# Optimization experiments

Hardware: AMD Instinct MI355X
Metric: run time of the kernel (lower is better)

Reference implementation:

```python
import jax, jax.numpy as jnp
import numpy as np


def setup_inputs() -> dict:
    key = jax.random.key(0)
    k1, k2, k3, k4, k5, k6 = jax.random.split(key, 6)
    H = 1024
    B, La, Lq = 32, 512, 64
    # kaiming_uniform with a=sqrt(5) on [H,H]: bound = sqrt(6/((1+5)*H)) = 1/sqrt(H)
    bound = 1.0 / np.sqrt(H)
    return {
        "article_feature": jax.random.normal(k1, (B, La, H), dtype=jnp.float32),
        "query_op_feature": jax.random.normal(k2, (B, Lq, H), dtype=jnp.float32),
        "weight1_1": jax.random.uniform(k3, (H, H), minval=-bound, maxval=bound, dtype=jnp.float32),
        "weight1_2": jax.random.uniform(k4, (H, H), minval=-bound, maxval=bound, dtype=jnp.float32),
        "weight2_1": jax.random.uniform(k5, (H, H), minval=-bound, maxval=bound, dtype=jnp.float32),
        "weight2_2": jax.random.uniform(k6, (H, H), minval=-bound, maxval=bound, dtype=jnp.float32),
    }


def reference(article_feature, query_op_feature, weight1_1, weight1_2, weight2_1, weight2_2):
    # article_feature: [B, La, H], query_op_feature: [B, Lq, H]
    # aq_attention: softmax over Lq of (A @ W1_1) @ Q^T -> [B, La, Lq]
    aq_scores = jnp.einsum("bah,hk,bqk->baq", article_feature, weight1_1, query_op_feature)
    aq_attention = jax.nn.softmax(aq_scores, axis=2)
    # qa_attention: softmax over La of (Q @ W1_2) @ A^T -> [B, Lq, La]
    qa_scores = jnp.einsum("bqh,hk,bak->bqa", query_op_feature, weight1_2, article_feature)
    qa_attention = jax.nn.softmax(qa_scores, axis=2)
    # S_a: relu((aq_attention @ Q) @ W2_1) -> [B, La, H]
    S_a = jax.nn.relu(jnp.einsum("baq,bqh,hk->bak", aq_attention, query_op_feature, weight2_1))
    # S_q: relu((qa_attention @ A) @ W2_2) -> [B, Lq, H]
    S_q = jax.nn.relu(jnp.einsum("bqa,bah,hk->bqk", qa_attention, article_feature, weight2_2))
    S_aq = jnp.max(S_a, axis=1)  # [B, H]
    S_qa = jnp.max(S_q, axis=1)  # [B, H]
    g = jnp.float32(0.5)
    return g * S_aq + (1.0 - g) * S_qa
```

## Files before the change

kernel.cpp:

```cpp
#include <hip/hip_runtime.h>
#include <stdint.h>


using f16x8 = __attribute__((ext_vector_type(8))) _Float16;
using f32x4 = __attribute__((ext_vector_type(4))) float;
typedef const __attribute__((address_space(1))) void* gas_t;
typedef __attribute__((address_space(3))) void* las_t;

__device__ __forceinline__ unsigned short f2h(float x) {
  _Float16 h = (_Float16)x;
  return __builtin_bit_cast(unsigned short, h);
}


__global__ __launch_bounds__(256) void conv16(const float* __restrict__ in,
    unsigned short* __restrict__ hi)
{
  int i = blockIdx.x * 256 + threadIdx.x;
  float4 v = ((const float4*)in)[i];
  ushort4 h;
  h.x = f2h(v.x); h.y = f2h(v.y); h.z = f2h(v.z); h.w = f2h(v.w);
  ((ushort4*)hi)[i] = h;
}

__global__ __launch_bounds__(256) void prep_W(
    const float* __restrict__ W11, const float* __restrict__ W12,
    const float* __restrict__ W21, const float* __restrict__ W22,
    unsigned short* __restrict__ Wcat, unsigned short* __restrict__ W21T,
    unsigned short* __restrict__ W22T)
{
  __shared__ float tile[32][33];
  int z = blockIdx.z;
  const float* src = z == 0 ? W11 : z == 1 ? W12 : z == 2 ? W21 : W22;
  int r0 = blockIdx.y * 32, c0 = blockIdx.x * 32;
  int tx = threadIdx.x, ty = threadIdx.y;
  #pragma unroll
  for (int i = 0; i < 4; ++i) {
    int r = r0 + ty + i * 8;
    float v = src[(long)r * 1024 + c0 + tx];
    tile[ty + i * 8][tx] = v;
    if (z == 0) Wcat[(long)r * 1024 + c0 + tx] = f2h(v);
  }
  __syncthreads();
  if (z > 0) {
    #pragma unroll
    for (int i = 0; i < 4; ++i) {
      float v = tile[tx][ty + i * 8];
      long o = (long)(c0 + ty + i * 8) * 1024 + r0 + tx;
      if (z == 1)      Wcat[1048576 + o] = f2h(v);
      else if (z == 2) W21T[o] = f2h(v);
      else             W22T[o] = f2h(v);
    }
  }
}

template<int BM, int BN, int OUT, bool BF32>
__device__ __forceinline__ void gemm_body(
    char* smem, int bx, int by, int z,
    const unsigned short* __restrict__ Ah,
    const unsigned short* __restrict__ Bh, const float* __restrict__ Bf,
    float* __restrict__ Cf, unsigned short* __restrict__ Ch,
    int M, int N, int K, int ldA, int ldB, int ldC, long sA, long sB, long sC, int mtiles)
{
  constexpr int AB = BM * 64;
  constexpr int MI = BM / 32, NI = BN / 32;
  char* As = smem;
  char* Bs = smem + AB;

  const int m0 = by * BM, n0 = bx * BN;
  const int t = threadIdx.x, lane = t & 63;
  const int wid = t >> 6, wr = wid >> 1, wc = wid & 1;

  const unsigned short* Ab = Ah + (long)z * sA;
  const unsigned short* Bb = BF32 ? nullptr : Bh + (long)z * sB;
  const float* Bfb = BF32 ? Bf + (long)z * sB : nullptr;

  f32x4 acc[MI][NI];
  #pragma unroll
  for (int i = 0; i < MI; ++i)
    #pragma unroll
    for (int j = 0; j < NI; ++j)
      acc[i][j] = f32x4{0.f, 0.f, 0.f, 0.f};

  auto stage4k = [&](char* lbuf, const unsigned short* g, int ld, int row0, int k0, int rmax) {
    int ob = t * 16;
    int e  = ob ^ (((ob >> 7) & 3) << 4);
    int m  = e >> 6, k = (e & 63) >> 1;
    int row = row0 + m; row = row < rmax ? row : rmax - 1;
    const unsigned short* gp = g + (long)row * ld + k0 + k;
    char* lp = lbuf + (t & ~63) * 16;
    __builtin_amdgcn_global_load_lds((gas_t)(const void*)gp, (las_t)(void*)lp, 16, 0, 0);
  };
  auto stageB_f32 = [&](char* lbuf, const float* g, int ld, int nb, int k0) {
    int ob = t * 16;
    int e  = ob ^ (((ob >> 7) & 3) << 4);
    int n  = e >> 6, kb = (e & 63) >> 1;
    f16x8 pk;
    #pragma unroll
    for (int j = 0; j < 8; ++j) {
      float v = g[(long)(k0 + kb + j) * ld + nb + n];
      pk[j] = (_Float16)v;
    }
    *(f16x8*)(lbuf + ob) = pk;
  };
  auto ldfrag = [&](const char* lbuf, int rr) -> f16x8 {
    int ob = rr * 64 + (lane >> 4) * 16;
    ob ^= ((ob >> 7) & 3) << 4;
    return *(const f16x8*)(lbuf + ob);
  };

  for (int k0 = 0; k0 < K; k0 += 32) {
    stage4k(As, Ab, ldA, m0, k0, M);
    if (BM == 128) stage4k(As + 4096, Ab, ldA, m0 + 64, k0, M);
    if (BF32) {
      stageB_f32(Bs, Bfb, ldB, n0, k0);
    } else {
      stage4k(Bs, Bb, ldB, n0, k0, N);
      if (BN == 128) stage4k(Bs + 4096, Bb, ldB, n0 + 64, k0, N);
    }
    __syncthreads();

    f16x8 ah[MI];
    #pragma unroll
    for (int mi = 0; mi < MI; ++mi)
      ah[mi] = ldfrag(As, wr * (BM / 2) + mi * 16 + (lane & 15));
    #pragma unroll
    for (int ni = 0; ni < NI; ++ni) {
      f16x8 bh = ldfrag(Bs, wc * (BN / 2) + ni * 16 + (lane & 15));
      #pragma unroll
      for (int mi = 0; mi < MI; ++mi)
        acc[mi][ni] = __builtin_amdgcn_mfma_f32_16x16x32_f16(ah[mi], bh, acc[mi][ni], 0, 0, 0);
    }
    __syncthreads();
  }

  if (OUT == 4 || OUT == 5) {
    float* red = (float*)smem;
    #pragma unroll
    for (int ni = 0; ni < NI; ++ni) {
      float pm = 0.0f;
      #pragma unroll
      for (int mi = 0; mi < MI; ++mi)
        #pragma unroll
        for (int r = 0; r < 4; ++r)
          pm = fmaxf(pm, acc[mi][ni][r]);
      int g = wr * 4 + (lane >> 4);
      int col = wc * (BN / 2) + ni * 16 + (lane & 15);
      red[g * BN + col] = pm;
    }
    __syncthreads();
    if (OUT == 4) {
      if (t < BN) {
        float m = red[t];
        #pragma unroll
        for (int g = 1; g < 8; ++g) m = fmaxf(m, red[g * BN + t]);
        Cf[(long)(z * mtiles + by) * ldC + n0 + t] = m;
      }
    } else {
      constexpr int NGR = BM / 64, PG = 8 / NGR;
      if (t < NGR * BN) {
        int hh = t / BN, col = t - hh * BN;
        float m = red[(hh * PG) * BN + col];
        #pragma unroll
        for (int i = 1; i < PG; ++i) m = fmaxf(m, red[(hh * PG + i) * BN + col]);
        Cf[(long)((m0 >> 6) + hh) * ldC + n0 + col] = m;
      }
    }
    return;
  }

  #pragma unroll
  for (int mi = 0; mi < MI; ++mi) {
    #pragma unroll
    for (int r = 0; r < 4; ++r) {
      int grow = m0 + wr * (BM / 2) + mi * 16 + (lane >> 4) * 4 + r;
      #pragma unroll
      for (int ni = 0; ni < NI; ++ni) {
        int gcol = n0 + wc * (BN / 2) + ni * 16 + (lane & 15);
        float v = acc[mi][ni][r];
        if (OUT == 1) {
          int b = grow >> 6, q = grow & 63;
          long dst = (long)b * 131072 + (long)((gcol >> 10) * 64 + q) * 1024 + (gcol & 1023);
          Ch[dst] = f2h(v);
        } else if (OUT == 2) {
          if (grow < M) Ch[(long)z * sC + (long)grow * ldC + gcol] = f2h(v);
        } else if (OUT == 3) {
          long dst = (long)(grow >> 6) * 65536 + (long)gcol * 64 + (grow & 63);
          Ch[dst] = f2h(v);
        }
      }
    }
  }
}


__global__ __launch_bounds__(256) void g1_kernel(
    const unsigned short* Q_hi, const unsigned short* Wcat, const unsigned short* W21T,
    unsigned short* Pcat, unsigned short* P3T)
{
  __shared__ char smem[12288];
  int bid = blockIdx.x;
  if (bid < 512) {
    gemm_body<128, 64, 1, false>(smem, bid & 31, bid >> 5, 0,
        Q_hi, Wcat, nullptr, nullptr, Pcat,
        2048, 2048, 1024, 1024, 1024, 0, 0, 0, 0, 0);
  } else {
    int b2 = bid - 512;
    gemm_body<128, 64, 3, false>(smem, b2 & 15, b2 >> 4, 0,
        Q_hi, W21T, nullptr, nullptr, P3T,
        2048, 1024, 1024, 1024, 1024, 0, 0, 0, 0, 0);
  }
}


__global__ __launch_bounds__(512) void g2_kernel(
    const float* __restrict__ Afeat, const unsigned short* __restrict__ Pcat,
    float* __restrict__ Spar)
{
  __shared__ char smem[12288];
  char* Ash = smem;
  char* Bs  = smem + 4096;

  int orig = blockIdx.x;
  int xcd = orig & 7, idx = orig >> 3;
  int z   = xcd * 4 + (idx >> 4);
  int sub = idx & 15;
  int by  = sub >> 1, kh = sub & 1;
  const int m0 = by * 64, kb = kh * 512;
  const int t = threadIdx.x, lane = t & 63;
  const int wid = t >> 6, wr = wid >> 1, wc = wid & 1;

  const float* Ab = Afeat + (long)z * 524288;
  const unsigned short* Bbh = Pcat + (long)z * 131072;

  f32x4 acc[4];
  #pragma unroll
  for (int i = 0; i < 4; ++i) acc[i] = f32x4{0.f, 0.f, 0.f, 0.f};

  auto ldfrag = [&](const char* lbuf, int rr) -> f16x8 {
    int ob = rr * 64 + (lane >> 4) * 16;
    ob ^= ((ob >> 7) & 3) << 4;
    return *(const f16x8*)(lbuf + ob);
  };

  for (int k0 = kb; k0 < kb + 512; k0 += 32) {
    {
      int ob = t * 8;
      int e  = ob ^ (((ob >> 7) & 3) << 4);
      int m  = e >> 6, ke = (e & 63) >> 1;
      float4 v = *(const float4*)(Ab + (long)(m0 + m) * 1024 + k0 + ke);
      ushort4 h;
      h.x = f2h(v.x); h.y = f2h(v.y); h.z = f2h(v.z); h.w = f2h(v.w);
      *(ushort4*)(Ash + ob) = h;
    }
    {
      int ob = t * 16;
      int e  = ob ^ (((ob >> 7) & 3) << 4);
      int n  = e >> 6, kk = (e & 63) >> 1;
      const unsigned short* gp = Bbh + (long)n * 1024 + k0 + kk;
      char* lp = Bs + (t & ~63) * 16;
      __builtin_amdgcn_global_load_lds((gas_t)(const void*)gp, (las_t)(void*)lp, 16, 0, 0);
    }
    __syncthreads();

    f16x8 ah = ldfrag(Ash, wr * 16 + (lane & 15));
    #pragma unroll
    for (int ni = 0; ni < 4; ++ni) {
      f16x8 bh = ldfrag(Bs, wc * 64 + ni * 16 + (lane & 15));
      acc[ni] = __builtin_amdgcn_mfma_f32_16x16x32_f16(ah, bh, acc[ni], 0, 0, 0);
    }
    __syncthreads();
  }

  float* dst = Spar + (long)kh * 2097152 + (long)z * 65536;
  #pragma unroll
  for (int r = 0; r < 4; ++r) {
    int grow = m0 + wr * 16 + (lane >> 4) * 4 + r;
    long base = (long)grow * 128 + wc * 64 + (lane & 15);
    dst[base]      = acc[0][r];
    dst[base + 16] = acc[1][r];
    dst[base + 32] = acc[2][r];
    dst[base + 48] = acc[3][r];
  }
}


__global__ __launch_bounds__(256) void softmax_both(const float* __restrict__ Sp,
    unsigned short* __restrict__ aq, unsigned short* __restrict__ qa)
{
  if (blockIdx.x < 4096) {
    int row  = blockIdx.x * 4 + (threadIdx.x >> 6);
    int lane = threadIdx.x & 63;
    long o = (long)row * 128 + lane;
    float v = Sp[o] + Sp[o + 2097152];
    float m = v;
    #pragma unroll
    for (int off = 32; off; off >>= 1) m = fmaxf(m, __shfl_xor(m, off));
    float e = __expf(v - m);
    float s = e;
    #pragma unroll
    for (int off = 32; off; off >>= 1) s += __shfl_xor(s, off);
    aq[(long)row * 64 + lane] = f2h(e / s);
  } else {
    int bq = blockIdx.x - 4096;
    int b = bq >> 6, q = bq & 63;
    int t = threadIdx.x;
    const float* base = Sp + (long)b * 65536 + 64 + q;
    float v0 = base[(long)t * 128]         + base[(long)t * 128 + 2097152];
    float v1 = base[(long)(t + 256) * 128] + base[(long)(t + 256) * 128 + 2097152];
    float m = fmaxf(v0, v1);
    #pragma unroll
    for (int off = 32; off; off >>= 1) m = fmaxf(m, __shfl_xor(m, off));
    __shared__ float sm[4], ss[4];
    int wid = t >> 6, lane = t & 63;
    if (lane == 0) sm[wid] = m;
    __syncthreads();
    float M = fmaxf(fmaxf(sm[0], sm[1]), fmaxf(sm[2], sm[3]));
    float e0 = __expf(v0 - M), e1 = __expf(v1 - M);
    float s = e0 + e1;
    #pragma unroll
    for (int off = 32; off; off >>= 1) s += __shfl_xor(s, off);
    if (lane == 0) ss[wid] = s;
    __syncthreads();
    float inv = 1.0f / ((ss[0] + ss[1]) + (ss[2] + ss[3]));
    qa[(long)bq * 512 + t]       = f2h(e0 * inv);
    qa[(long)bq * 512 + t + 256] = f2h(e1 * inv);
  }
}


__global__ __launch_bounds__(256) void g3_kernel(
    const unsigned short* aq, const unsigned short* P3T, float* PmaxA,
    const unsigned short* qa, const float* Afeat, unsigned short* ctx)
{
  __shared__ char smem[16384];
  int bid = blockIdx.x;
  if (bid < 1024) {
    gemm_body<128, 128, 4, false>(smem, bid & 7, (bid >> 3) & 3, bid >> 5,
        aq, P3T, nullptr, PmaxA, nullptr,
        512, 1024, 64, 64, 64, 1024, 32768L, 65536L, 0, 4);
  } else {
    int b2 = bid - 1024;
    gemm_body<64, 64, 2, true>(smem, b2 & 15, 0, b2 >> 4,
        qa, nullptr, Afeat, nullptr, ctx,
        64, 1024, 512, 512, 1024, 1024, 32768L, 524288L, 65536L, 0);
  }
}


__global__ __launch_bounds__(256) void g4_kernel(
    const unsigned short* ctx, const unsigned short* W22T, float* PmaxQ)
{
  __shared__ char smem[8192];
  gemm_body<64, 64, 5, false>(smem, blockIdx.x, blockIdx.y, 0,
      ctx, W22T, nullptr, PmaxQ, nullptr,
      2048, 1024, 1024, 1024, 1024, 1024, 0, 0, 0, 0);
}

__global__ __launch_bounds__(256) void final_combine(
    const float* __restrict__ PmaxA, const float* __restrict__ PmaxQ, float* __restrict__ out)
{
  int idx = blockIdx.x * 256 + threadIdx.x;
  int b = idx >> 10, h = idx & 1023;
  float m = PmaxA[(long)(b * 4) * 1024 + h];
  #pragma unroll
  for (int mt = 1; mt < 4; ++mt)
    m = fmaxf(m, PmaxA[(long)(b * 4 + mt) * 1024 + h]);
  out[idx] = 0.5f * m + 0.5f * PmaxQ[idx];
}


extern "C" void kernel_launch(void* const* d_in, const int* in_sizes, int n_in,
                              void* d_out, int out_size, void* d_ws, size_t ws_size,
                              hipStream_t stream) {
  const float* Afeat = (const float*)d_in[0];
  const float* Qfeat = (const float*)d_in[1];
  const float* W11   = (const float*)d_in[2];
  const float* W12   = (const float*)d_in[3];
  const float* W21   = (const float*)d_in[4];
  const float* W22   = (const float*)d_in[5];
  float* out = (float*)d_out;

  char* w = (char*)d_ws;
  auto alloc = [&](long bytes) { char* p = w; w += bytes; return p; };
  unsigned short* Q_hi  = (unsigned short*)alloc(4194304);
  unsigned short* Wcat  = (unsigned short*)alloc(4194304);
  unsigned short* W21T  = (unsigned short*)alloc(2097152);
  unsigned short* W22T  = (unsigned short*)alloc(2097152);
  unsigned short* Pcat  = (unsigned short*)alloc(8388608);
  unsigned short* P3T   = (unsigned short*)alloc(4194304);
  float*          Spar  = (float*)alloc(16777216);
  unsigned short* aq    = (unsigned short*)alloc(2097152);
  unsigned short* qa    = (unsigned short*)alloc(2097152);
  unsigned short* ctx   = (unsigned short*)alloc(4194304);
  float*          PmaxA = (float*)alloc(524288);
  float*          PmaxQ = (float*)alloc(131072);

  dim3 blk(256), tblk(32, 8);

  conv16<<<2048, blk, 0, stream>>>(Qfeat, Q_hi);
  prep_W<<<dim3(32, 32, 4), tblk, 0, stream>>>(W11, W12, W21, W22, Wcat, W21T, W22T);

  g1_kernel<<<768, blk, 0, stream>>>(Q_hi, Wcat, W21T, Pcat, P3T);
  g2_kernel<<<512, dim3(512), 0, stream>>>(Afeat, Pcat, Spar);
  softmax_both<<<6144, blk, 0, stream>>>(Spar, aq, qa);
  g3_kernel<<<1536, blk, 0, stream>>>(aq, P3T, PmaxA, qa, Afeat, ctx);
  g4_kernel<<<dim3(16, 32), blk, 0, stream>>>(ctx, W22T, PmaxQ);
  final_combine<<<128, blk, 0, stream>>>(PmaxA, PmaxQ, out);
}
```

Before: 110.4 us.

## Fuse prep kernels, final combine into g4, and stage two K-chunks per sync

Merges the Q fp16 conversion into the weight-prep launch and folds the final max/combine into the g4 epilogue, which removes two kernel launches. The GEMM main loops in gemm_body and g2 now stage two 32-wide K slices per iteration, halving the number of barrier pairs. The cost is doubled shared memory per block, which may lower occupancy. The g4 epilogue now also reads PmaxA and writes the output directly.

```diff
diff --git a/kernel.cpp b/kernel.cpp
--- a/kernel.cpp
+++ b/kernel.cpp
@@ -13,27 +13,27 @@
 }
 
 
-__global__ __launch_bounds__(256) void conv16(const float* __restrict__ in,
-    unsigned short* __restrict__ hi)
-{
-  int i = blockIdx.x * 256 + threadIdx.x;
-  float4 v = ((const float4*)in)[i];
-  ushort4 h;
-  h.x = f2h(v.x); h.y = f2h(v.y); h.z = f2h(v.z); h.w = f2h(v.w);
-  ((ushort4*)hi)[i] = h;
-}
-
-__global__ __launch_bounds__(256) void prep_W(
+__global__ __launch_bounds__(256) void prep_all(
     const float* __restrict__ W11, const float* __restrict__ W12,
     const float* __restrict__ W21, const float* __restrict__ W22,
+    const float* __restrict__ Qfeat,
     unsigned short* __restrict__ Wcat, unsigned short* __restrict__ W21T,
-    unsigned short* __restrict__ W22T)
-{
+    unsigned short* __restrict__ W22T, unsigned short* __restrict__ Q_hi)
+{
+  int z = blockIdx.z;
+  int tx = threadIdx.x, ty = threadIdx.y;
+  if (z >= 4) {
+    int blk = (z - 4) * 1024 + blockIdx.y * 32 + blockIdx.x;
+    int i = blk * 256 + ty * 32 + tx;
+    float4 v = ((const float4*)Qfeat)[i];
+    ushort4 h;
+    h.x = f2h(v.x); h.y = f2h(v.y); h.z = f2h(v.z); h.w = f2h(v.w);
+    ((ushort4*)Q_hi)[i] = h;
+    return;
+  }
   __shared__ float tile[32][33];
-  int z = blockIdx.z;
   const float* src = z == 0 ? W11 : z == 1 ? W12 : z == 2 ? W21 : W22;
   int r0 = blockIdx.y * 32, c0 = blockIdx.x * 32;
-  int tx = threadIdx.x, ty = threadIdx.y;
   #pragma unroll
   for (int i = 0; i < 4; ++i) {
     int r = r0 + ty + i * 8;
@@ -62,10 +62,12 @@
     float* __restrict__ Cf, unsigned short* __restrict__ Ch,
     int M, int N, int K, int ldA, int ldB, int ldC, long sA, long sB, long sC, int mtiles)
 {
-  constexpr int AB = BM * 64;
+  constexpr int ACH = BM * 64, BCH = BN * 64;
   constexpr int MI = BM / 32, NI = BN / 32;
-  char* As = smem;
-  char* Bs = smem + AB;
+  char* As0 = smem;
+  char* As1 = smem + ACH;
+  char* Bs0 = smem + 2 * ACH;
+  char* Bs1 = Bs0 + BCH;
 
   const int m0 = by * BM, n0 = bx * BN;
   const int t = threadIdx.x, lane = t & 63;
@@ -108,33 +110,41 @@
     ob ^= ((ob >> 7) & 3) << 4;
     return *(const f16x8*)(lbuf + ob);
   };
-
-  for (int k0 = 0; k0 < K; k0 += 32) {
-    stage4k(As, Ab, ldA, m0, k0, M);
-    if (BM == 128) stage4k(As + 4096, Ab, ldA, m0 + 64, k0, M);
-    if (BF32) {
-      stageB_f32(Bs, Bfb, ldB, n0, k0);
-    } else {
-      stage4k(Bs, Bb, ldB, n0, k0, N);
-      if (BN == 128) stage4k(Bs + 4096, Bb, ldB, n0 + 64, k0, N);
-    }
-    __syncthreads();
-
+  auto compute32 = [&](const char* Ac, const char* Bc) {
     f16x8 ah[MI];
     #pragma unroll
     for (int mi = 0; mi < MI; ++mi)
-      ah[mi] = ldfrag(As, wr * (BM / 2) + mi * 16 + (lane & 15));
+      ah[mi] = ldfrag(Ac, wr * (BM / 2) + mi * 16 + (lane & 15));
     #pragma unroll
     for (int ni = 0; ni < NI; ++ni) {
-      f16x8 bh = ldfrag(Bs, wc * (BN / 2) + ni * 16 + (lane & 15));
+      f16x8 bh = ldfrag(Bc, wc * (BN / 2) + ni * 16 + (lane & 15));
       #pragma unroll
       for (int mi = 0; mi < MI; ++mi)
         acc[mi][ni] = __builtin_amdgcn_mfma_f32_16x16x32_f16(ah[mi], bh, acc[mi][ni], 0, 0, 0);
     }
-    __syncthreads();
-  }
-
-  if (OUT == 4 || OUT == 5) {
+  };
+
+  for (int k0 = 0; k0 < K; k0 += 64) {
+    stage4k(As0, Ab, ldA, m0, k0, M);
+    if (BM == 128) stage4k(As0 + 4096, Ab, ldA, m0 + 64, k0, M);
+    stage4k(As1, Ab, ldA, m0, k0 + 32, M);
+    if (BM == 128) stage4k(As1 + 4096, Ab, ldA, m0 + 64, k0 + 32, M);
+    if (BF32) {
+      stageB_f32(Bs0, Bfb, ldB, n0, k0);
+      stageB_f32(Bs1, Bfb, ldB, n0, k0 + 32);
+    } else {
+      stage4k(Bs0, Bb, ldB, n0, k0, N);
+      if (BN == 128) stage4k(Bs0 + 4096, Bb, ldB, n0 + 64, k0, N);
+      stage4k(Bs1, Bb, ldB, n0, k0 + 32, N);
+      if (BN == 128) stage4k(Bs1 + 4096, Bb, ldB, n0 + 64, k0 + 32, N);
+    }
+    __syncthreads();
+    compute32(As0, Bs0);
+    compute32(As1, Bs1);
+    __syncthreads();
+  }
+
+  if (OUT == 4 || OUT == 6) {
     float* red = (float*)smem;
     #pragma unroll
     for (int ni = 0; ni < NI; ++ni) {
@@ -157,13 +167,15 @@
         Cf[(long)(z * mtiles + by) * ldC + n0 + t] = m;
       }
     } else {
-      constexpr int NGR = BM / 64, PG = 8 / NGR;
-      if (t < NGR * BN) {
-        int hh = t / BN, col = t - hh * BN;
-        float m = red[(hh * PG) * BN + col];
+      if (t < BN) {
+        float pq = red[t];
         #pragma unroll
-        for (int i = 1; i < PG; ++i) m = fmaxf(m, red[(hh * PG + i) * BN + col]);
-        Cf[(long)((m0 >> 6) + hh) * ldC + n0 + col] = m;
+        for (int g = 1; g < 8; ++g) pq = fmaxf(pq, red[g * BN + t]);
+        float pa = Bf[(long)(by * 4) * 1024 + n0 + t];
+        #pragma unroll
+        for (int mt = 1; mt < 4; ++mt)
+          pa = fmaxf(pa, Bf[(long)(by * 4 + mt) * 1024 + n0 + t]);
+        Cf[(long)by * 1024 + n0 + t] = 0.5f * pa + 0.5f * pq;
       }
     }
     return;
@@ -198,7 +210,7 @@
     const unsigned short* Q_hi, const unsigned short* Wcat, const unsigned short* W21T,
     unsigned short* Pcat, unsigned short* P3T)
 {
-  __shared__ char smem[12288];
+  __shared__ char smem[24576];
   int bid = blockIdx.x;
   if (bid < 512) {
     gemm_body<128, 64, 1, false>(smem, bid & 31, bid >> 5, 0,
@@ -217,9 +229,11 @@
     const float* __restrict__ Afeat, const unsigned short* __restrict__ Pcat,
     float* __restrict__ Spar)
 {
-  __shared__ char smem[12288];
-  char* Ash = smem;
-  char* Bs  = smem + 4096;
+  __shared__ char smem[24576];
+  char* Ash0 = smem;
+  char* Ash1 = smem + 4096;
+  char* Bs0  = smem + 8192;
+  char* Bs1  = smem + 16384;
 
   int orig = blockIdx.x;
   int xcd = orig & 7, idx = orig >> 3;
@@ -242,33 +256,40 @@
     ob ^= ((ob >> 7) & 3) << 4;
     return *(const f16x8*)(lbuf + ob);
   };
-
-  for (int k0 = kb; k0 < kb + 512; k0 += 32) {
-    {
-      int ob = t * 8;
-      int e  = ob ^ (((ob >> 7) & 3) << 4);
-      int m  = e >> 6, ke = (e & 63) >> 1;
-      float4 v = *(const float4*)(Ab + (long)(m0 + m) * 1024 + k0 + ke);
-      ushort4 h;
-      h.x = f2h(v.x); h.y = f2h(v.y); h.z = f2h(v.z); h.w = f2h(v.w);
-      *(ushort4*)(Ash + ob) = h;
-    }
-    {
-      int ob = t * 16;
-      int e  = ob ^ (((ob >> 7) & 3) << 4);
-      int n  = e >> 6, kk = (e & 63) >> 1;
-      const unsigned short* gp = Bbh + (long)n * 1024 + k0 + kk;
-      char* lp = Bs + (t & ~63) * 16;
-      __builtin_amdgcn_global_load_lds((gas_t)(const void*)gp, (las_t)(void*)lp, 16, 0, 0);
-    }
-    __syncthreads();
-
-    f16x8 ah = ldfrag(Ash, wr * 16 + (lane & 15));
+  auto stageA = [&](char* lbuf, int k0) {
+    int ob = t * 8;
+    int e  = ob ^ (((ob >> 7) & 3) << 4);
+    int m  = e >> 6, ke = (e & 63) >> 1;
+    float4 v = *(const float4*)(Ab + (long)(m0 + m) * 1024 + k0 + ke);
+    ushort4 h;
+    h.x = f2h(v.x); h.y = f2h(v.y); h.z = f2h(v.z); h.w = f2h(v.w);
+    *(ushort4*)(lbuf + ob) = h;
+  };
+  auto stageB = [&](char* lbuf, int k0) {
+    int ob = t * 16;
+    int e  = ob ^ (((ob >> 7) & 3) << 4);
+    int n  = e >> 6, kk = (e & 63) >> 1;
+    const unsigned short* gp = Bbh + (long)n * 1024 + k0 + kk;
+    char* lp = lbuf + (t & ~63) * 16;
+    __builtin_amdgcn_global_load_lds((gas_t)(const void*)gp, (las_t)(void*)lp, 16, 0, 0);
+  };
+  auto compute32 = [&](const char* Ac, const char* Bc) {
+    f16x8 ah = ldfrag(Ac, wr * 16 + (lane & 15));
     #pragma unroll
     for (int ni = 0; ni < 4; ++ni) {
-      f16x8 bh = ldfrag(Bs, wc * 64 + ni * 16 + (lane & 15));
+      f16x8 bh = ldfrag(Bc, wc * 64 + ni * 16 + (lane & 15));
       acc[ni] = __builtin_amdgcn_mfma_f32_16x16x32_f16(ah, bh, acc[ni], 0, 0, 0);
     }
+  };
+
+  for (int k0 = kb; k0 < kb + 512; k0 += 64) {
+    stageA(Ash0, k0);
+    stageA(Ash1, k0 + 32);
+    stageB(Bs0, k0);
+    stageB(Bs1, k0 + 32);
+    __syncthreads();
+    compute32(Ash0, Bs0);
+    compute32(Ash1, Bs1);
     __syncthreads();
   }
 
@@ -333,7 +354,7 @@
     const unsigned short* aq, const unsigned short* P3T, float* PmaxA,
     const unsigned short* qa, const float* Afeat, unsigned short* ctx)
 {
-  __shared__ char smem[16384];
+  __shared__ char smem[32768];
   int bid = blockIdx.x;
   if (bid < 1024) {
     gemm_body<128, 128, 4, false>(smem, bid & 7, (bid >> 3) & 3, bid >> 5,
@@ -349,24 +370,13 @@
 
 
 __global__ __launch_bounds__(256) void g4_kernel(
-    const unsigned short* ctx, const unsigned short* W22T, float* PmaxQ)
-{
-  __shared__ char smem[8192];
-  gemm_body<64, 64, 5, false>(smem, blockIdx.x, blockIdx.y, 0,
-      ctx, W22T, nullptr, PmaxQ, nullptr,
+    const unsigned short* ctx, const unsigned short* W22T,
+    const float* PmaxA, float* out)
+{
+  __shared__ char smem[16384];
+  gemm_body<64, 64, 6, false>(smem, blockIdx.x, blockIdx.y, 0,
+      ctx, W22T, PmaxA, out, nullptr,
       2048, 1024, 1024, 1024, 1024, 1024, 0, 0, 0, 0);
-}
-
-__global__ __launch_bounds__(256) void final_combine(
-    const float* __restrict__ PmaxA, const float* __restrict__ PmaxQ, float* __restrict__ out)
-{
-  int idx = blockIdx.x * 256 + threadIdx.x;
-  int b = idx >> 10, h = idx & 1023;
-  float m = PmaxA[(long)(b * 4) * 1024 + h];
-  #pragma unroll
-  for (int mt = 1; mt < 4; ++mt)
-    m = fmaxf(m, PmaxA[(long)(b * 4 + mt) * 1024 + h]);
-  out[idx] = 0.5f * m + 0.5f * PmaxQ[idx];
 }
 
 
@@ -394,17 +404,14 @@
   unsigned short* qa    = (unsigned short*)alloc(2097152);
   unsigned short* ctx   = (unsigned short*)alloc(4194304);
   float*          PmaxA = (float*)alloc(524288);
-  float*          PmaxQ = (float*)alloc(131072);
 
   dim3 blk(256), tblk(32, 8);
 
-  conv16<<<2048, blk, 0, stream>>>(Qfeat, Q_hi);
-  prep_W<<<dim3(32, 32, 4), tblk, 0, stream>>>(W11, W12, W21, W22, Wcat, W21T, W22T);
-
+  prep_all<<<dim3(32, 32, 6), tblk, 0, stream>>>(W11, W12, W21, W22, Qfeat,
+                                                 Wcat, W21T, W22T, Q_hi);
   g1_kernel<<<768, blk, 0, stream>>>(Q_hi, Wcat, W21T, Pcat, P3T);
   g2_kernel<<<512, dim3(512), 0, stream>>>(Afeat, Pcat, Spar);
   softmax_both<<<6144, blk, 0, stream>>>(Spar, aq, qa);
   g3_kernel<<<1536, blk, 0, stream>>>(aq, P3T, PmaxA, qa, Afeat, ctx);
-  g4_kernel<<<dim3(16, 32), blk, 0, stream>>>(ctx, W22T, PmaxQ);
-  final_combine<<<128, blk, 0, stream>>>(PmaxA, PmaxQ, out);
-}
+  g4_kernel<<<dim3(16, 32), blk, 0, stream>>>(ctx, W22T, PmaxA, out);
+}
```

Result: faster. 102.0 us (-7.6%).
